# Performance work log

Measured on AMD Instinct MI355X. Metric: run time of the kernel, lower is better.

Reference implementation:

```python
import jax, jax.numpy as jnp
import numpy as np

PATCH = 9  # patch_size (kernel_size=1, stride=1, padding=0, dilation_patch=1)


def setup_inputs() -> dict:
    key = jax.random.key(0)
    k1, k2 = jax.random.split(key)
    B, C, H, W = 4, 256, 128, 128
    return {
        "input1": jax.random.normal(k1, (B, C, H, W), dtype=jnp.float32),
        "input2": jax.random.normal(k2, (B, C, H, W), dtype=jnp.float32),
    }


def _correlation(input1, input2, patch=PATCH):
    # Faithful to torch _correlation_patch_based fast path:
    # corr[b, dy*P+dx, h, w] = sum_c input1[b,c,h,w] * input2_pad[b,c,h+dy,w+dx]
    # where input2 is zero-padded by P//2 (matches F.unfold padding=P//2).
    B, C, H, W = input1.shape
    pad = patch // 2
    i2p = jnp.pad(input2, ((0, 0), (0, 0), (pad, pad), (pad, pad)))
    # displacement offsets in unfold order: ky-major, kx-minor
    offs = jnp.stack(
        jnp.meshgrid(jnp.arange(patch), jnp.arange(patch), indexing="ij"), axis=-1
    ).reshape(-1, 2)  # (P*P, 2)

    def body(carry, off):
        # shifted window of input2, same (B,C,H,W) footprint (no unfold blowup)
        win = jax.lax.dynamic_slice(i2p, (0, 0, off[0], off[1]), (B, C, H, W))
        return carry, jnp.einsum("bchw,bchw->bhw", input1, win)

    _, corr = jax.lax.scan(body, None, offs)  # (P*P, B, H, W)
    return jnp.transpose(corr, (1, 0, 2, 3))  # (B, P*P, H, W)


def reference(input1, input2):
    return _correlation(input1, input2)
```

## Files before the change

kernel.cpp:

```cpp
#include <hip/hip_runtime.h>

#define BB   4
#define CC   256
#define HH   128
#define WW   128
#define PAD  4
#define KOUT 81

#define TH   4
#define SW   16
#define KC   32
#define NCHUNK (CC / KC)
#define AK   40
#define BROWS (TH + 8)

typedef _Float16 half8 __attribute__((ext_vector_type(8)));
typedef float    f32x4 __attribute__((ext_vector_type(4)));

__global__ __launch_bounds__(512, 4)
void corr_mfma6(const float* __restrict__ i1,
                const float* __restrict__ i2,
                float* __restrict__ out)
{
    __shared__ __align__(16) _Float16 Ald[64 * AK];
    __shared__ __align__(16) _Float16 Bld[384 * AK];

    const int t    = threadIdx.x;
    const int wave = t >> 6;
    const int lane = t & 63;
    const int l15  = lane & 15;
    const int quad = lane >> 4;
    const int wr   = wave >> 1;
    const int wd   = wave & 1;

    const int raw     = blockIdx.x + 8 * blockIdx.y + 256 * blockIdx.z;
    const int logical = (raw & 7) * 128 + (raw >> 3);
    const int b  = logical >> 8;
    const int h0 = ((logical >> 3) & 31) * TH;
    const int w0 = (logical & 7) * SW;

    const size_t strideC = (size_t)HH * WW;
    const float* i1b = i1 + (size_t)b * CC * strideC;
    const float* i2b = i2 + (size_t)b * CC * strideC;

    bool stager, valid;
    const float* gp;
    _Float16* ld0;

    if (t < 288) {
        stager = true;
        const int g   = t % 6;
        const int t6  = t / 6;
        const int ch8 = t6 & 3;
        const int sr  = t6 >> 2;
        const int row  = h0 - PAD + sr;
        const int col0 = w0 - PAD + 4 * g;
        valid = (row >= 0) && (row < HH) && (col0 >= 0) && (col0 + 3 < WW);
        gp  = i2b + (size_t)(valid ? row : 0) * WW + (valid ? col0 : 0)
                  + (size_t)ch8 * 8 * strideC;
        ld0 = &Bld[(sr * 32 + 4 * g) * AK + ch8 * 8];
    } else if (t < 352) {
        stager = true;
        const int i   = t - 288;
        const int g   = i & 3;
        const int t4  = i >> 2;
        const int ch8 = t4 & 3;
        const int sr  = t4 >> 2;
        valid = true;
        gp  = i1b + (size_t)(h0 + sr) * WW + (w0 + 4 * g)
                  + (size_t)ch8 * 8 * strideC;
        ld0 = &Ald[(sr * 16 + 4 * g) * AK + ch8 * 8];
    } else {
        stager = false;
        valid  = false;
        gp  = i1b;
        ld0 = &Ald[0];
    }

    f32x4 acc[5][2];
#pragma unroll
    for (int j = 0; j < 5; ++j) {
        acc[j][0] = (f32x4){0.f, 0.f, 0.f, 0.f};
        acc[j][1] = (f32x4){0.f, 0.f, 0.f, 0.f};
    }

    f32x4 L[8];

    if (valid) {
#pragma unroll
        for (int j = 0; j < 8; ++j)
            L[j] = *(const f32x4*)(gp + (size_t)j * strideC);
#pragma unroll
        for (int i = 0; i < 4; ++i) {
            half8 hv;
#pragma unroll
            for (int k = 0; k < 8; ++k) hv[k] = (_Float16)L[k][i];
            *(half8*)(ld0 + i * AK) = hv;
        }
    } else if (stager) {
        const half8 z = (half8){0, 0, 0, 0, 0, 0, 0, 0};
#pragma unroll
        for (int i = 0; i < 4; ++i)
            *(half8*)(ld0 + i * AK) = z;
    }
    __syncthreads();

#pragma unroll 1
    for (int ch = 0; ch < NCHUNK; ++ch) {
        const bool more = (ch + 1 < NCHUNK);

        if (valid && more) {
            const float* g = gp + (size_t)(ch + 1) * KC * strideC;
#pragma unroll
            for (int j = 0; j < 8; ++j)
                L[j] = *(const f32x4*)(g + (size_t)j * strideC);
        }

        {
            const half8 a = *(const half8*)&Ald[(wr * 16 + l15) * AK + quad * 8];
            if (wd == 0) {
#pragma unroll
                for (int j = 0; j < 5; ++j) {
                    const int r = wr + j;
                    const half8 b0 = *(const half8*)&Bld[(r * 32 + l15) * AK + quad * 8];
                    acc[j][0] = __builtin_amdgcn_mfma_f32_16x16x32_f16(a, b0, acc[j][0], 0, 0, 0);
                    const half8 b1 = *(const half8*)&Bld[(r * 32 + 16 + l15) * AK + quad * 8];
                    acc[j][1] = __builtin_amdgcn_mfma_f32_16x16x32_f16(a, b1, acc[j][1], 0, 0, 0);
                }
            } else {
#pragma unroll
                for (int j = 0; j < 4; ++j) {
                    const int r = wr + 5 + j;
                    const half8 b0 = *(const half8*)&Bld[(r * 32 + l15) * AK + quad * 8];
                    acc[j][0] = __builtin_amdgcn_mfma_f32_16x16x32_f16(a, b0, acc[j][0], 0, 0, 0);
                    const half8 b1 = *(const half8*)&Bld[(r * 32 + 16 + l15) * AK + quad * 8];
                    acc[j][1] = __builtin_amdgcn_mfma_f32_16x16x32_f16(a, b1, acc[j][1], 0, 0, 0);
                }
            }
        }

        if (more) {
            __syncthreads();
            if (valid) {
#pragma unroll
                for (int i = 0; i < 4; ++i) {
                    half8 hv;
#pragma unroll
                    for (int k = 0; k < 8; ++k) hv[k] = (_Float16)L[k][i];
                    *(half8*)(ld0 + i * AK) = hv;
                }
            }
            __syncthreads();
        }
    }

    const int h = h0 + wr;
    if (wd == 0) {
#pragma unroll
        for (int j = 0; j < 5; ++j) {
            const int dy = j;
#pragma unroll
            for (int tt = 0; tt < 2; ++tt) {
#pragma unroll
                for (int reg = 0; reg < 4; ++reg) {
                    const int p  = quad * 4 + reg;
                    const int dx = l15 + 16 * tt - p;
                    if (dx >= 0 && dx <= 8) {
                        out[(((size_t)b * KOUT + (dy * 9 + dx)) * HH + h) * WW + (w0 + p)] =
                            acc[j][tt][reg];
                    }
                }
            }
        }
    } else {
#pragma unroll
        for (int j = 0; j < 4; ++j) {
            const int dy = 5 + j;
#pragma unroll
            for (int tt = 0; tt < 2; ++tt) {
#pragma unroll
                for (int reg = 0; reg < 4; ++reg) {
                    const int p  = quad * 4 + reg;
                    const int dx = l15 + 16 * tt - p;
                    if (dx >= 0 && dx <= 8) {
                        out[(((size_t)b * KOUT + (dy * 9 + dx)) * HH + h) * WW + (w0 + p)] =
                            acc[j][tt][reg];
                    }
                }
            }
        }
    }
}

extern "C" void kernel_launch(void* const* d_in, const int* in_sizes, int n_in,
                              void* d_out, int out_size, void* d_ws, size_t ws_size,
                              hipStream_t stream)
{
    (void)in_sizes; (void)n_in; (void)d_ws; (void)ws_size; (void)out_size;
    const float* i1 = (const float*)d_in[0];
    const float* i2 = (const float*)d_in[1];
    float* out = (float*)d_out;

    dim3 grid(WW / SW, HH / TH, BB);
    dim3 block(512);
    corr_mfma6<<<grid, block, 0, stream>>>(i1, i2, out);
}
```

Measured before the change: 190.0 us.

## Double-buffer LDS with smaller channel chunks and 16x16x16 MFMA

Halves the channel chunk to 16, switches to the 16x16x16 f16 MFMA, and double-buffers the staged fp16 tiles in LDS so the next chunk's conversion overlaps compute. This cuts each iteration from two barriers to one and keeps two global loads in flight per stager. The cost is twice as many iterations and smaller MFMA ops, so more barriers and instructions overall. A custom barrier waits only on lgkmcnt.

```diff
diff --git a/kernel.cpp b/kernel.cpp
--- a/kernel.cpp
+++ b/kernel.cpp
@@ -9,21 +9,76 @@
 
 #define TH   4
 #define SW   16
-#define KC   32
+#define KC   16
 #define NCHUNK (CC / KC)
-#define AK   40
-#define BROWS (TH + 8)
-
-typedef _Float16 half8 __attribute__((ext_vector_type(8)));
+#define AK   20
+#define ABASE 0
+#define BBASE (64 * AK)
+#define LDSH  (BBASE + 384 * AK)
+
+typedef _Float16 half4 __attribute__((ext_vector_type(4)));
 typedef float    f32x4 __attribute__((ext_vector_type(4)));
 
+#define MFMA16(a, b, c) __builtin_amdgcn_mfma_f32_16x16x16f16((a), (b), (c), 0, 0, 0)
+
+#define BARRIER() do {                                        \
+    asm volatile("s_waitcnt lgkmcnt(0)" ::: "memory");        \
+    __builtin_amdgcn_s_barrier();                             \
+    asm volatile("" ::: "memory");                            \
+} while (0)
+
+__device__ __forceinline__ void issue4(f32x4 (&L)[4], const float* g, size_t strideC)
+{
+    L[0] = *(const f32x4*)(g);
+    L[1] = *(const f32x4*)(g + strideC);
+    L[2] = *(const f32x4*)(g + 2 * strideC);
+    L[3] = *(const f32x4*)(g + 3 * strideC);
+}
+
+__device__ __forceinline__ void convert4(const f32x4 (&L)[4], _Float16* dst)
+{
+#pragma unroll
+    for (int i = 0; i < 4; ++i) {
+        half4 hv;
+        hv[0] = (_Float16)L[0][i];
+        hv[1] = (_Float16)L[1][i];
+        hv[2] = (_Float16)L[2][i];
+        hv[3] = (_Float16)L[3][i];
+        *(half4*)(dst + i * AK) = hv;
+    }
+}
+
+__device__ __forceinline__ void compute_chunk(const _Float16* buf, f32x4 (&acc)[5][2],
+                                              int wr, int wd, int l15, int quad)
+{
+    const half4 a = *(const half4*)&buf[ABASE + (wr * 16 + l15) * AK + quad * 4];
+    if (wd == 0) {
+#pragma unroll
+        for (int j = 0; j < 5; ++j) {
+            const int r = wr + j;
+            const half4 b0 = *(const half4*)&buf[BBASE + (r * 32 + l15) * AK + quad * 4];
+            acc[j][0] = MFMA16(a, b0, acc[j][0]);
+            const half4 b1 = *(const half4*)&buf[BBASE + (r * 32 + 16 + l15) * AK + quad * 4];
+            acc[j][1] = MFMA16(a, b1, acc[j][1]);
+        }
+    } else {
+#pragma unroll
+        for (int j = 0; j < 4; ++j) {
+            const int r = wr + 5 + j;
+            const half4 b0 = *(const half4*)&buf[BBASE + (r * 32 + l15) * AK + quad * 4];
+            acc[j][0] = MFMA16(a, b0, acc[j][0]);
+            const half4 b1 = *(const half4*)&buf[BBASE + (r * 32 + 16 + l15) * AK + quad * 4];
+            acc[j][1] = MFMA16(a, b1, acc[j][1]);
+        }
+    }
+}
+
 __global__ __launch_bounds__(512, 4)
-void corr_mfma6(const float* __restrict__ i1,
+void corr_mfma7(const float* __restrict__ i1,
                 const float* __restrict__ i2,
                 float* __restrict__ out)
 {
-    __shared__ __align__(16) _Float16 Ald[64 * AK];
-    __shared__ __align__(16) _Float16 Bld[384 * AK];
+    __shared__ _Float16 lds[2][LDSH];
 
     const int t    = threadIdx.x;
     const int wave = t >> 6;
@@ -45,37 +100,38 @@
 
     bool stager, valid;
     const float* gp;
-    _Float16* ld0;
+    int ldoff;
 
     if (t < 288) {
         stager = true;
         const int g   = t % 6;
         const int t6  = t / 6;
-        const int ch8 = t6 & 3;
+        const int ch4 = t6 & 3;
         const int sr  = t6 >> 2;
         const int row  = h0 - PAD + sr;
         const int col0 = w0 - PAD + 4 * g;
         valid = (row >= 0) && (row < HH) && (col0 >= 0) && (col0 + 3 < WW);
-        gp  = i2b + (size_t)(valid ? row : 0) * WW + (valid ? col0 : 0)
-                  + (size_t)ch8 * 8 * strideC;
-        ld0 = &Bld[(sr * 32 + 4 * g) * AK + ch8 * 8];
+        gp = i2b + (size_t)(valid ? row : 0) * WW + (valid ? col0 : 0)
+                 + (size_t)ch4 * 4 * strideC;
+        ldoff = BBASE + (sr * 32 + 4 * g) * AK + ch4 * 4;
     } else if (t < 352) {
         stager = true;
         const int i   = t - 288;
         const int g   = i & 3;
         const int t4  = i >> 2;
-        const int ch8 = t4 & 3;
+        const int ch4 = t4 & 3;
         const int sr  = t4 >> 2;
         valid = true;
-        gp  = i1b + (size_t)(h0 + sr) * WW + (w0 + 4 * g)
-                  + (size_t)ch8 * 8 * strideC;
-        ld0 = &Ald[(sr * 16 + 4 * g) * AK + ch8 * 8];
+        gp = i1b + (size_t)(h0 + sr) * WW + (w0 + 4 * g)
+                 + (size_t)ch4 * 4 * strideC;
+        ldoff = ABASE + (sr * 16 + 4 * g) * AK + ch4 * 4;
     } else {
         stager = false;
         valid  = false;
-        gp  = i1b;
-        ld0 = &Ald[0];
-    }
+        gp    = i1b;
+        ldoff = 0;
+    }
+    const bool sv = stager && valid;
 
     f32x4 acc[5][2];
 #pragma unroll
@@ -84,73 +140,41 @@
         acc[j][1] = (f32x4){0.f, 0.f, 0.f, 0.f};
     }
 
-    f32x4 L[8];
-
-    if (valid) {
-#pragma unroll
-        for (int j = 0; j < 8; ++j)
-            L[j] = *(const f32x4*)(gp + (size_t)j * strideC);
+    f32x4 La[4], Lb[4];
+
+    if (stager && !valid) {
+        const half4 z = (half4){0, 0, 0, 0};
 #pragma unroll
         for (int i = 0; i < 4; ++i) {
-            half8 hv;
-#pragma unroll
-            for (int k = 0; k < 8; ++k) hv[k] = (_Float16)L[k][i];
-            *(half8*)(ld0 + i * AK) = hv;
-        }
-    } else if (stager) {
-        const half8 z = (half8){0, 0, 0, 0, 0, 0, 0, 0};
-#pragma unroll
-        for (int i = 0; i < 4; ++i)
-            *(half8*)(ld0 + i * AK) = z;
-    }
-    __syncthreads();
+            *(half4*)(&lds[0][ldoff + i * AK]) = z;
+            *(half4*)(&lds[1][ldoff + i * AK]) = z;
+        }
+    }
+    if (sv) {
+        issue4(La, gp, strideC);
+        issue4(Lb, gp + (size_t)KC * strideC, strideC);
+        convert4(La, &lds[0][ldoff]);
+    }
+    BARRIER();
 
 #pragma unroll 1
-    for (int ch = 0; ch < NCHUNK; ++ch) {
-        const bool more = (ch + 1 < NCHUNK);
-
-        if (valid && more) {
-            const float* g = gp + (size_t)(ch + 1) * KC * strideC;
-#pragma unroll
-            for (int j = 0; j < 8; ++j)
-                L[j] = *(const f32x4*)(g + (size_t)j * strideC);
-        }
-
-        {
-            const half8 a = *(const half8*)&Ald[(wr * 16 + l15) * AK + quad * 8];
-            if (wd == 0) {
-#pragma unroll
-                for (int j = 0; j < 5; ++j) {
-                    const int r = wr + j;
-                    const half8 b0 = *(const half8*)&Bld[(r * 32 + l15) * AK + quad * 8];
-                    acc[j][0] = __builtin_amdgcn_mfma_f32_16x16x32_f16(a, b0, acc[j][0], 0, 0, 0);
-                    const half8 b1 = *(const half8*)&Bld[(r * 32 + 16 + l15) * AK + quad * 8];
-                    acc[j][1] = __builtin_amdgcn_mfma_f32_16x16x32_f16(a, b1, acc[j][1], 0, 0, 0);
-                }
-            } else {
-#pragma unroll
-                for (int j = 0; j < 4; ++j) {
-                    const int r = wr + 5 + j;
-                    const half8 b0 = *(const half8*)&Bld[(r * 32 + l15) * AK + quad * 8];
-                    acc[j][0] = __builtin_amdgcn_mfma_f32_16x16x32_f16(a, b0, acc[j][0], 0, 0, 0);
-                    const half8 b1 = *(const half8*)&Bld[(r * 32 + 16 + l15) * AK + quad * 8];
-                    acc[j][1] = __builtin_amdgcn_mfma_f32_16x16x32_f16(a, b1, acc[j][1], 0, 0, 0);
-                }
-            }
-        }
-
-        if (more) {
-            __syncthreads();
-            if (valid) {
-#pragma unroll
-                for (int i = 0; i < 4; ++i) {
-                    half8 hv;
-#pragma unroll
-                    for (int k = 0; k < 8; ++k) hv[k] = (_Float16)L[k][i];
-                    *(half8*)(ld0 + i * AK) = hv;
-                }
-            }
-            __syncthreads();
+    for (int jp = 0; jp < 8; ++jp) {
+        const int j = 2 * jp;
+
+        if (sv && (j + 2 < NCHUNK))
+            issue4(La, gp + (size_t)(j + 2) * KC * strideC, strideC);
+        compute_chunk(&lds[0][0], acc, wr, wd, l15, quad);
+        if (sv)
+            convert4(Lb, &lds[1][ldoff]);
+        BARRIER();
+
+        if (sv && (j + 3 < NCHUNK))
+            issue4(Lb, gp + (size_t)(j + 3) * KC * strideC, strideC);
+        compute_chunk(&lds[1][0], acc, wr, wd, l15, quad);
+        if (jp < 7) {
+            if (sv)
+                convert4(La, &lds[0][ldoff]);
+            BARRIER();
         }
     }
 
@@ -203,5 +227,5 @@
 
     dim3 grid(WW / SW, HH / TH, BB);
     dim3 block(512);
-    corr_mfma6<<<grid, block, 0, stream>>>(i1, i2, out);
-}
+    corr_mfma7<<<grid, block, 0, stream>>>(i1, i2, out);
+}
```

Measured after the change: 185.3 us. 1.03x faster.
